# Optimization experiments

Hardware: AMD Instinct MI355X
Metric: run time of the kernel (lower is better)

## Reference

```python
import jax, jax.numpy as jnp
import numpy as np

NQ = 14            # n_qubits
NB = 2             # n_blocks
KLOC = 4           # k_local
K = 2 ** KLOC      # Hermitian observable dim = 16
NOFF = K * (K - 1) // 2   # 120 off-diagonal params
DEPTH = 3          # vqc_depth
IN_DIM = 784
OUT_DIM = 10
BATCH = 128
GROUPS = [list(range(s, s + KLOC)) for s in range(NQ - KLOC + 1)]  # sliding k-local groups
NOBS = len(GROUPS)  # 11
TOTAL_ENC = NB * ((NQ // 2) + ((NQ - 1) // 2)) * 15  # 390 SU(4) encoding params

# 15 two-qubit Pauli words in PennyLane's lexicographic IXYZ order (identity excluded)
_I = np.eye(2, dtype=np.complex64)
_X = np.array([[0, 1], [1, 0]], np.complex64)
_Y = np.array([[0, -1j], [1j, 0]], np.complex64)
_Z = np.array([[1, 0], [0, -1]], np.complex64)
_P = {'I': _I, 'X': _X, 'Y': _Y, 'Z': _Z}
_WORDS = [a + b for a in 'IXYZ' for b in 'IXYZ'][1:]
P15 = jnp.asarray(np.stack([np.kron(_P[w[0]], _P[w[1]]) for w in _WORDS]))  # (15,4,4)
CNOT = jnp.asarray(np.array([[1, 0, 0, 0], [0, 1, 0, 0], [0, 0, 0, 1], [0, 0, 1, 0]], np.complex64))
_ROWS, _COLS = np.tril_indices(K, -1)  # row-major lower-tri order == create_Hermitian fill order


def su4(theta):
    """PennyLane SpecialUnitary: U = expm(i * sum_m theta_m P_m), theta: (B,15).
    The generator is Hermitian, so use eigh instead of generic expm."""
    Hm = jnp.einsum('bm,mij->bij', theta.astype(jnp.complex64), P15)  # (B,4,4) Hermitian
    w, V = jnp.linalg.eigh(Hm)
    return jnp.einsum('bij,bj,bkj->bik', V, jnp.exp(1j * w.astype(jnp.complex64)), V.conj())


def apply_gate(state, U, wires):
    """Apply a k-qubit gate U ((B,2^k,2^k) or (2^k,2^k)) to state (B, 2,...,2)."""
    n = state.ndim - 1
    k = len(wires)
    axes = [w + 1 for w in wires]
    perm = [0] + axes + [a for a in range(1, n + 1) if a not in axes]
    st = jnp.transpose(state, perm)
    shp = st.shape
    st = st.reshape(shp[0], 2 ** k, -1)
    if U.ndim == 3:
        st = jnp.einsum('bij,bjr->bir', U, st)
    else:
        st = jnp.einsum('ij,bjr->bir', U, st)
    return jnp.transpose(st.reshape(shp), np.argsort(perm))


def expval_herm(state, H, wires):
    """<psi| H_{wires} |psi> per batch element."""
    n = state.ndim - 1
    axes = [w + 1 for w in wires]
    perm = [0] + axes + [a for a in range(1, n + 1) if a not in axes]
    st = jnp.transpose(state, perm).reshape(state.shape[0], H.shape[0], -1)
    return jnp.einsum('bkr,kl,blr->b', st.conj(), H, st).real


def create_hermitian(A, Bp, D):
    """Faithful port of create_Hermitian: lower-tri A+iB (row-major), diag D[1:] on
    positions 0..K-2 (D[0] unused, last diag 0), then H = h + h^dagger (diag doubled)."""
    h = jnp.zeros((K, K), jnp.complex64).at[_ROWS, _COLS].set(A + 1j * Bp)
    d = jnp.zeros((K,), A.dtype).at[jnp.arange(K - 1)].set(D[1:])
    h = h + jnp.diag(d).astype(jnp.complex64)
    return h + h.conj().T


def ry_mat(theta):
    c = jnp.cos(theta / 2)
    s = jnp.sin(theta / 2)
    return jnp.stack([jnp.stack([c, -s]), jnp.stack([s, c])]).astype(jnp.complex64)


def setup_inputs():
    key = jax.random.key(0)
    ks = jax.random.split(key, 9)
    lim = 1.0 / np.sqrt(IN_DIM)
    lim_h = 1.0 / np.sqrt(NOBS)
    return {
        'x': jax.random.normal(ks[0], (BATCH, IN_DIM), jnp.float32),
        'W_enc': jax.random.uniform(ks[1], (TOTAL_ENC, IN_DIM), jnp.float32, -lim, lim),
        'b_enc': jax.random.uniform(ks[2], (TOTAL_ENC,), jnp.float32, -lim, lim),
        'var_params': 0.01 * jax.random.normal(ks[3], (DEPTH, NQ), jnp.float32),
        'A': 2.0 * jax.random.normal(ks[4], (NOBS, NOFF), jnp.float32),
        'Bp': 2.0 * jax.random.normal(ks[5], (NOBS, NOFF), jnp.float32),
        'D': 2.0 * jax.random.normal(ks[6], (NOBS, K), jnp.float32),
        'W_head': jax.random.uniform(ks[7], (OUT_DIM, NOBS), jnp.float32, -lim_h, lim_h),
        'b_head': jax.random.uniform(ks[8], (OUT_DIM,), jnp.float32, -lim_h, lim_h),
    }


def reference(x, W_enc, b_enc, var_params, A, Bp, D, W_head, b_head):
    encoded = x @ W_enc.T + b_enc                      # (B, 390)
    Hs = jax.vmap(create_hermitian)(A, Bp, D)          # (NOBS, K, K)
    Bsz = x.shape[0]
    state = jnp.zeros((Bsz,) + (2,) * NQ, jnp.complex64).at[(slice(None),) + (0,) * NQ].set(1.0)
    # SU(4) brick-layer encoding: even pairs then odd pairs per block
    idx = 0
    for _ in range(NB):
        for q in list(range(0, NQ - 1, 2)) + list(range(1, NQ - 1, 2)):
            state = apply_gate(state, su4(encoded[:, idx:idx + 15]), [q, q + 1])
            idx += 15
    # variational RY + CNOT brick layers
    for layer in range(DEPTH):
        for q in range(NQ):
            state = apply_gate(state, ry_mat(var_params[layer, q]), [q])
        for q in list(range(0, NQ - 1, 2)) + list(range(1, NQ - 1, 2)):
            state = apply_gate(state, CNOT, [q, q + 1])
    q_out = jnp.stack([expval_herm(state, Hs[w], GROUPS[w]) for w in range(NOBS)], axis=1)
    q_out = q_out.astype(jnp.float32)                  # (B, NOBS)
    return q_out @ W_head.T + b_head                   # (B, OUT_DIM)
```

## Files before the change

kernel.cpp:

```cpp
#include <hip/hip_runtime.h>
#include <math.h>

#define NQ      14
#define NSTATE  16384
#define BATCH   128
#define DEPTH   3
#define NOBS    11
#define KDIM    16
#define NOFF    120
#define INDIM   784
#define OUTDIM  10

__device__ __forceinline__ int F2(int a) { return a + (a >> 4); }
#define PHYS2 (NSTATE + (NSTATE >> 4))

__device__ __forceinline__ float sbc(float x) {
  return __int_as_float(__builtin_amdgcn_readfirstlane(__float_as_int(x)));
}

__global__ __launch_bounds__(256) void enc_kernel(
    const float* __restrict__ x, const float* __restrict__ W,
    const float* __restrict__ bvec, float* __restrict__ theta)
{
  int wave = ((blockIdx.x << 2) | (threadIdx.x >> 6));
  int lane = threadIdx.x & 63;
  int g = wave >> 7;
  int b = wave & 127;

  const float4* x4 = (const float4*)(x + (size_t)b * INDIM);
  const float4* w4 = (const float4*)(W + (size_t)g * 15 * INDIM);

  float acc[15];
#pragma unroll
  for (int m = 0; m < 15; ++m) acc[m] = 0.f;
#pragma unroll
  for (int it = 0; it < 4; ++it) {
    int j4 = lane + it * 64;
    if (j4 < 196) {
      float4 xv = x4[j4];
#pragma unroll
      for (int m = 0; m < 15; ++m) {
        float4 wv = w4[m * 196 + j4];
        acc[m] = fmaf(xv.x, wv.x, fmaf(xv.y, wv.y, fmaf(xv.z, wv.z, fmaf(xv.w, wv.w, acc[m]))));
      }
    }
  }
#pragma unroll
  for (int m = 0; m < 15; ++m) {
#pragma unroll
    for (int off = 32; off; off >>= 1) acc[m] += __shfl_xor(acc[m], off);
  }
  if (lane == 0) {
#pragma unroll
    for (int m = 0; m < 15; ++m) theta[(size_t)wave * 15 + m] = acc[m] + bvec[g * 15 + m];
  }
}

__global__ __launch_bounds__(256) void expm_kernel(
    const float* __restrict__ theta, float2* __restrict__ Ubuf)
{
  int gid  = blockIdx.x * 256 + threadIdx.x;
  int pair = gid >> 2;
  int j    = gid & 3;
  int lane = threadIdx.x & 63;
  int grp  = lane & 60;

  const float* th = theta + (size_t)pair * 15;

  const float pr_[4][4] = {{1,0,0,1},{0,1,1,0},{0,0,0,0},{1,0,0,-1}};
  const float pi_[4][4] = {{0,0,0,0},{0,0,0,0},{0,-1,1,0},{0,0,0,0}};

  float Hre[16], Him[16];
#pragma unroll
  for (int e = 0; e < 16; ++e) { Hre[e] = 0.f; Him[e] = 0.f; }
  float tsum = 0.f;
#pragma unroll
  for (int m = 0; m < 15; ++m) {
    float tv = th[m];
    tsum += fabsf(tv);
    const int code = m + 1;
    const int a = code >> 2, c = code & 3;
#pragma unroll
    for (int i = 0; i < 4; ++i)
#pragma unroll
      for (int jj = 0; jj < 4; ++jj) {
        float ar = pr_[a][(i >> 1) * 2 + (jj >> 1)], ai = pi_[a][(i >> 1) * 2 + (jj >> 1)];
        float br = pr_[c][(i & 1) * 2 + (jj & 1)],   bi = pi_[c][(i & 1) * 2 + (jj & 1)];
        Hre[i * 4 + jj] += tv * (ar * br - ai * bi);
        Him[i * 4 + jj] += tv * (ar * bi + ai * br);
      }
  }
  int s = 0;
  if (tsum > 0.25f) {
    s = (int)ceilf(log2f(tsum * 4.0f));
    if (s < 0) s = 0;
    if (s > 14) s = 14;
  }
  float sc = exp2f((float)(-s));
  float Gre[16], Gim[16];
#pragma unroll
  for (int e = 0; e < 16; ++e) { Gre[e] = -Him[e] * sc; Gim[e] = Hre[e] * sc; }

  float Tcr[4], Tci[4];
#pragma unroll
  for (int i = 0; i < 4; ++i) {
    Tcr[i] = Gre[i * 4 + j] * (1.f / 9.f) + ((i == j) ? 1.f : 0.f);
    Tci[i] = Gim[i * 4 + j] * (1.f / 9.f);
  }
#pragma unroll
  for (int k = 8; k >= 1; --k) {
    float nr[4], ni[4];
    float invk = 1.0f / (float)k;
#pragma unroll
    for (int i = 0; i < 4; ++i) {
      float xr = 0.f, xi = 0.f;
#pragma unroll
      for (int l = 0; l < 4; ++l) {
        xr = fmaf(Gre[i * 4 + l], Tcr[l], fmaf(-Gim[i * 4 + l], Tci[l], xr));
        xi = fmaf(Gre[i * 4 + l], Tci[l], fmaf( Gim[i * 4 + l], Tcr[l], xi));
      }
      nr[i] = invk * xr + ((i == j) ? 1.f : 0.f);
      ni[i] = invk * xi;
    }
#pragma unroll
    for (int i = 0; i < 4; ++i) { Tcr[i] = nr[i]; Tci[i] = ni[i]; }
  }
  for (int it = 0; it < s; ++it) {
    float nr[4] = {0.f, 0.f, 0.f, 0.f}, ni[4] = {0.f, 0.f, 0.f, 0.f};
#pragma unroll
    for (int l = 0; l < 4; ++l) {
      int src = grp | l;
      float tlr = Tcr[l], tli = Tci[l];
#pragma unroll
      for (int i = 0; i < 4; ++i) {
        float br = __shfl(Tcr[i], src);
        float bi = __shfl(Tci[i], src);
        nr[i] = fmaf(br, tlr, fmaf(-bi, tli, nr[i]));
        ni[i] = fmaf(br, tli, fmaf( bi, tlr, ni[i]));
      }
    }
#pragma unroll
    for (int i = 0; i < 4; ++i) { Tcr[i] = nr[i]; Tci[i] = ni[i]; }
  }
#pragma unroll
  for (int i = 0; i < 4; ++i)
    Ubuf[(size_t)pair * 16 + i * 4 + j] = make_float2(Tcr[i], Tci[i]);
}

template<int S>
__device__ __forceinline__ int grpbase(int t) {
  return ((t >> S) << (S + 4)) | (t & ((1 << S) - 1));
}
template<int S>
__device__ __forceinline__ void ldgrp(const float2* st, int base, float* vr, float* vi) {
#pragma unroll
  for (int k = 0; k < 16; ++k) {
    float2 v = st[F2(base + (k << S))];
    vr[k] = v.x; vi[k] = v.y;
  }
}
template<int S>
__device__ __forceinline__ void stgrp(float2* st, int base, const float* vr, const float* vi) {
#pragma unroll
  for (int k = 0; k < 16; ++k) st[F2(base + (k << S))] = make_float2(vr[k], vi[k]);
}
__device__ __forceinline__ int base2s(int t) {
  return ((t >> 7) << 11) | (((t >> 5) & 3) << 7) | (t & 31);
}
__device__ __forceinline__ int addr2s(int base, int k) {
  return base + ((k >> 2) << 9) + ((k & 3) << 5);
}
__device__ __forceinline__ void ldgrp2(const float2* st, int base, float* vr, float* vi) {
#pragma unroll
  for (int k = 0; k < 16; ++k) {
    float2 v = st[F2(addr2s(base, k))];
    vr[k] = v.x; vi[k] = v.y;
  }
}
__device__ __forceinline__ void stgrp2(float2* st, int base, const float* vr, const float* vi) {
#pragma unroll
  for (int k = 0; k < 16; ++k) st[F2(addr2s(base, k))] = make_float2(vr[k], vi[k]);
}

__device__ __forceinline__ void loadU(const float2* __restrict__ Ug, float* ur, float* ui) {
#pragma unroll
  for (int e = 0; e < 16; ++e) {
    float2 u = Ug[e];
    ur[e] = sbc(u.x); ui[e] = sbc(u.y);
  }
}

__device__ __forceinline__ void applyU_hi(float* vr, float* vi, const float* ur, const float* ui) {
#pragma unroll
  for (int j2 = 0; j2 < 4; ++j2) {
    float ar[4], ai[4];
#pragma unroll
    for (int j = 0; j < 4; ++j) { ar[j] = vr[4 * j + j2]; ai[j] = vi[4 * j + j2]; }
#pragma unroll
    for (int i = 0; i < 4; ++i) {
      float xr = 0.f, xi = 0.f;
#pragma unroll
      for (int j = 0; j < 4; ++j) {
        xr = fmaf(ur[4 * i + j], ar[j], fmaf(-ui[4 * i + j], ai[j], xr));
        xi = fmaf(ur[4 * i + j], ai[j], fmaf( ui[4 * i + j], ar[j], xi));
      }
      vr[4 * i + j2] = xr; vi[4 * i + j2] = xi;
    }
  }
}
__device__ __forceinline__ void applyU_lo(float* vr, float* vi, const float* ur, const float* ui) {
#pragma unroll
  for (int i2 = 0; i2 < 4; ++i2) {
    float ar[4], ai[4];
#pragma unroll
    for (int j = 0; j < 4; ++j) { ar[j] = vr[4 * i2 + j]; ai[j] = vi[4 * i2 + j]; }
#pragma unroll
    for (int i = 0; i < 4; ++i) {
      float xr = 0.f, xi = 0.f;
#pragma unroll
      for (int j = 0; j < 4; ++j) {
        xr = fmaf(ur[4 * i + j], ar[j], fmaf(-ui[4 * i + j], ai[j], xr));
        xi = fmaf(ur[4 * i + j], ai[j], fmaf( ui[4 * i + j], ar[j], xi));
      }
      vr[4 * i2 + i] = xr; vi[4 * i2 + i] = xi;
    }
  }
}
__device__ __forceinline__ void applyU_mid(float* vr, float* vi, const float* ur, const float* ui) {
#pragma unroll
  for (int o = 0; o < 4; ++o) {
    const int kb = ((o >> 1) << 3) | (o & 1);
    float ar[4], ai[4];
#pragma unroll
    for (int j = 0; j < 4; ++j) { ar[j] = vr[kb | (j << 1)]; ai[j] = vi[kb | (j << 1)]; }
#pragma unroll
    for (int i = 0; i < 4; ++i) {
      float xr = 0.f, xi = 0.f;
#pragma unroll
      for (int j = 0; j < 4; ++j) {
        xr = fmaf(ur[4 * i + j], ar[j], fmaf(-ui[4 * i + j], ai[j], xr));
        xi = fmaf(ur[4 * i + j], ai[j], fmaf( ui[4 * i + j], ar[j], xi));
      }
      vr[kb | (i << 1)] = xr; vi[kb | (i << 1)] = xi;
    }
  }
}

template<int B>
__device__ __forceinline__ void ry16(float* vr, float* vi, float c, float s) {
#pragma unroll
  for (int k = 0; k < 16; ++k) {
    if (!(k & (1 << B))) {
      const int k1 = k | (1 << B);
      float r0 = vr[k], i0 = vi[k], r1 = vr[k1], i1 = vi[k1];
      vr[k]  = fmaf(c, r0, -s * r1);  vi[k]  = fmaf(c, i0, -s * i1);
      vr[k1] = fmaf(s, r0,  c * r1);  vi[k1] = fmaf(s, i0,  c * i1);
    }
  }
}
template<int CB, int TB>
__device__ __forceinline__ void cx16(float* vr, float* vi) {
#pragma unroll
  for (int k = 0; k < 16; ++k) {
    if ((k & (1 << CB)) && !(k & (1 << TB))) {
      const int k1 = k | (1 << TB);
      float tr = vr[k]; vr[k] = vr[k1]; vr[k1] = tr;
      float ti = vi[k]; vi[k] = vi[k1]; vi[k1] = ti;
    }
  }
}

template<int S>
__device__ __forceinline__ void enc_pass3(float2* st, const float2* __restrict__ U,
                                          int gHi, int gLo, int gMid, int b, int t) {
  float ur[16], ui[16], vr[16], vi[16];
  int base = grpbase<S>(t);
  ldgrp<S>(st, base, vr, vi);
  loadU(U + ((size_t)gHi  * BATCH + b) * 16, ur, ui); applyU_hi (vr, vi, ur, ui);
  loadU(U + ((size_t)gLo  * BATCH + b) * 16, ur, ui); applyU_lo (vr, vi, ur, ui);
  loadU(U + ((size_t)gMid * BATCH + b) * 16, ur, ui); applyU_mid(vr, vi, ur, ui);
  stgrp<S>(st, base, vr, vi);
}
__device__ __forceinline__ void enc_passD(float2* st, const float2* __restrict__ U,
                                          int gLo, int gMid, int b, int t) {
  float ur[16], ui[16], vr[16], vi[16];
  int base = t << 4;
  ldgrp<0>(st, base, vr, vi);
  loadU(U + ((size_t)gLo  * BATCH + b) * 16, ur, ui); applyU_lo (vr, vi, ur, ui);
  loadU(U + ((size_t)gMid * BATCH + b) * 16, ur, ui); applyU_mid(vr, vi, ur, ui);
  stgrp<0>(st, base, vr, vi);
}
__device__ __forceinline__ void enc_passE(float2* st, const float2* __restrict__ U,
                                          int gA, int gB, int b, int t) {
  float ur[16], ui[16], vr[16], vi[16];
  int base = base2s(t);
  ldgrp2(st, base, vr, vi);
  loadU(U + ((size_t)gA * BATCH + b) * 16, ur, ui); applyU_hi(vr, vi, ur, ui);
  loadU(U + ((size_t)gB * BATCH + b) * 16, ur, ui); applyU_lo(vr, vi, ur, ui);
  stgrp2(st, base, vr, vi);
}
template<int S>
__device__ __forceinline__ void var_pass3(float2* st, const float* __restrict__ vp,
                                          int l, int qbase, int t) {
  float vr[16], vi[16];
  int base = grpbase<S>(t);
  ldgrp<S>(st, base, vr, vi);
  float c[4], sn[4];
#pragma unroll
  for (int i = 0; i < 4; ++i) {
    float a = sbc(vp[l * NQ + qbase + i]) * 0.5f;
    c[i] = cosf(a); sn[i] = sinf(a);
  }
  ry16<3>(vr, vi, c[0], sn[0]);
  ry16<2>(vr, vi, c[1], sn[1]);
  ry16<1>(vr, vi, c[2], sn[2]);
  ry16<0>(vr, vi, c[3], sn[3]);
  cx16<3, 2>(vr, vi);
  cx16<1, 0>(vr, vi);
  cx16<2, 1>(vr, vi);
  stgrp<S>(st, base, vr, vi);
}
__device__ __forceinline__ void var_passD(float2* st, const float* __restrict__ vp,
                                          int l, int t) {
  float vr[16], vi[16];
  int base = t << 4;
  ldgrp<0>(st, base, vr, vi);
  float a0 = sbc(vp[l * NQ + 12]) * 0.5f;
  float a1 = sbc(vp[l * NQ + 13]) * 0.5f;
  ry16<1>(vr, vi, cosf(a0), sinf(a0));
  ry16<0>(vr, vi, cosf(a1), sinf(a1));
  cx16<1, 0>(vr, vi);
  cx16<2, 1>(vr, vi);
  stgrp<0>(st, base, vr, vi);
}
__device__ __forceinline__ void var_passE(float2* st, int t) {
  float vr[16], vi[16];
  int base = base2s(t);
  ldgrp2(st, base, vr, vi);
  cx16<3, 2>(vr, vi);
  cx16<1, 0>(vr, vi);
  stgrp2(st, base, vr, vi);
}

__global__ __launch_bounds__(1024) void qsim_kernel(
    const float2* __restrict__ U, const float* __restrict__ var_params,
    const float* __restrict__ A, const float* __restrict__ Bp,
    const float* __restrict__ D, const float* __restrict__ Wh,
    const float* __restrict__ bh, float* __restrict__ out)
{
  __shared__ float2 st[PHYS2];
  __shared__ float obsb[256];
  __shared__ float red[16];
  __shared__ float qv[NOBS];

  const int t = threadIdx.x;
  const int b = blockIdx.x;

  for (int i = t; i < PHYS2; i += 1024) st[i] = make_float2(0.f, 0.f);
  __syncthreads();
  if (t == 0) st[0] = make_float2(1.f, 0.f);
  __syncthreads();

  for (int nb = 0; nb < 2; ++nb) {
    int gI = nb * 13;
    enc_pass3<10>(st, U, gI + 0, gI + 1, gI + 7,  b, t); __syncthreads();
    enc_pass3<6 >(st, U, gI + 2, gI + 3, gI + 9,  b, t); __syncthreads();
    enc_pass3<2 >(st, U, gI + 4, gI + 5, gI + 11, b, t); __syncthreads();
    enc_passD    (st, U, gI + 6, gI + 12,         b, t); __syncthreads();
    enc_passE    (st, U, gI + 8, gI + 10,         b, t); __syncthreads();
  }

  for (int l = 0; l < DEPTH; ++l) {
    var_pass3<10>(st, var_params, l, 0, t); __syncthreads();
    var_pass3<6 >(st, var_params, l, 4, t); __syncthreads();
    var_pass3<2 >(st, var_params, l, 8, t); __syncthreads();
    var_passD    (st, var_params, l,    t); __syncthreads();
    var_passE    (st, t);                   __syncthreads();
  }

  for (int w = 0; w < NOBS; ++w) {
    if (t < NOFF) obsb[t] = A[w * NOFF + t];
    else if (t < 2 * NOFF) obsb[t] = Bp[w * NOFF + (t - NOFF)];
    else if (t < 2 * NOFF + KDIM) obsb[t] = D[w * KDIM + (t - 2 * NOFF)];
    __syncthreads();

    int shift = 10 - w;
    int hi = t >> shift;
    int lo = t & ((1 << shift) - 1);
    int base2 = (hi << (shift + 4)) | lo;
    float sr[16], si[16];
#pragma unroll
    for (int k = 0; k < 16; ++k) {
      float2 v = st[F2(base2 + (k << shift))];
      sr[k] = v.x; si[k] = v.y;
    }
    float E = 0.f;
#pragma unroll
    for (int k = 0; k < 15; ++k)
      E = fmaf(obsb[240 + k + 1], sr[k] * sr[k] + si[k] * si[k], E);
#pragma unroll
    for (int k = 1; k < 16; ++k) {
#pragma unroll
      for (int l2 = 0; l2 < k; ++l2) {
        const int pidx = (k * (k - 1)) / 2 + l2;
        float t1 = sr[k] * sr[l2] + si[k] * si[l2];
        float t2 = si[k] * sr[l2] - sr[k] * si[l2];
        E = fmaf(obsb[pidx], t1, fmaf(obsb[NOFF + pidx], t2, E));
      }
    }
    E *= 2.0f;
#pragma unroll
    for (int off = 32; off; off >>= 1) E += __shfl_xor(E, off);
    if ((t & 63) == 0) red[t >> 6] = E;
    __syncthreads();
    if (t == 0) {
      float sum = 0.f;
      for (int ww = 0; ww < 16; ++ww) sum += red[ww];
      qv[w] = sum;
    }
    __syncthreads();
  }

  if (t < OUTDIM) {
    float o = bh[t];
#pragma unroll
    for (int w = 0; w < NOBS; ++w) o = fmaf(Wh[t * NOBS + w], qv[w], o);
    out[b * OUTDIM + t] = o;
  }
}

extern "C" void kernel_launch(void* const* d_in, const int* in_sizes, int n_in,
                              void* d_out, int out_size, void* d_ws, size_t ws_size,
                              hipStream_t stream) {
  const float* x          = (const float*)d_in[0];
  const float* W_enc      = (const float*)d_in[1];
  const float* b_enc      = (const float*)d_in[2];
  const float* var_params = (const float*)d_in[3];
  const float* A          = (const float*)d_in[4];
  const float* Bp         = (const float*)d_in[5];
  const float* D          = (const float*)d_in[6];
  const float* W_head     = (const float*)d_in[7];
  const float* b_head     = (const float*)d_in[8];
  float* out = (float*)d_out;

  float*  theta = (float*)d_ws;
  size_t  thBytes = (size_t)3328 * 15 * sizeof(float);
  float2* Ubuf = (float2*)((char*)d_ws + ((thBytes + 255) / 256) * 256);

  enc_kernel <<<832, 256, 0, stream>>>(x, W_enc, b_enc, theta);
  expm_kernel<<<52,  256, 0, stream>>>(theta, Ubuf);
  qsim_kernel<<<128, 1024, 0, stream>>>(Ubuf, var_params, A, Bp, D,
                                        W_head, b_head, out);
}
```

Baseline: 207.4 us.

## Duplicate state simulation across two blocks per sample, split observables, atomically combine

Launches two blocks per batch element, each redoing the full state-vector simulation and then evaluating half of the 11 observables. Partial head outputs are combined with atomicAdd into an output zeroed by a memset. Observable parameters are preloaded once and the per-observable syncs are removed. The aim is to fill more of the GPU's CUs, at the cost of doubling the simulation work and adding a memset launch.

```diff
diff --git a/kernel.cpp b/kernel.cpp
--- a/kernel.cpp
+++ b/kernel.cpp
@@ -349,16 +349,16 @@
     const float* __restrict__ bh, float* __restrict__ out)
 {
   __shared__ float2 st[PHYS2];
-  __shared__ float obsb[256];
-  __shared__ float red[16];
-  __shared__ float qv[NOBS];
+  __shared__ float obsa[6 * 256];
+  __shared__ float red[6][16];
 
   const int t = threadIdx.x;
-  const int b = blockIdx.x;
-
-  for (int i = t; i < PHYS2; i += 1024) st[i] = make_float2(0.f, 0.f);
-  __syncthreads();
-  if (t == 0) st[0] = make_float2(1.f, 0.f);
+  const int b = blockIdx.x >> 1;
+  const int h = blockIdx.x & 1;
+  const int nw = h ? 5 : 6;
+
+  for (int i = t; i < PHYS2; i += 1024)
+    st[i] = (i == 0) ? make_float2(1.f, 0.f) : make_float2(0.f, 0.f);
   __syncthreads();
 
   for (int nb = 0; nb < 2; ++nb) {
@@ -378,16 +378,25 @@
     var_passE    (st, t);                   __syncthreads();
   }
 
-  for (int w = 0; w < NOBS; ++w) {
-    if (t < NOFF) obsb[t] = A[w * NOFF + t];
-    else if (t < 2 * NOFF) obsb[t] = Bp[w * NOFF + (t - NOFF)];
-    else if (t < 2 * NOFF + KDIM) obsb[t] = D[w * KDIM + (t - 2 * NOFF)];
-    __syncthreads();
-
+  for (int i = t; i < nw * 256; i += 1024) {
+    int idx = i >> 8, off = i & 255, w = 2 * idx + h;
+    float v;
+    if (off < NOFF)            v = A[w * NOFF + off];
+    else if (off < 2 * NOFF)   v = Bp[w * NOFF + (off - NOFF)];
+    else if (off < 2 * NOFF + KDIM) v = D[w * KDIM + (off - 2 * NOFF)];
+    else v = 0.f;
+    obsa[i] = v;
+  }
+  __syncthreads();
+
+  const int wave = t >> 6;
+  for (int idx = 0; idx < nw; ++idx) {
+    const int w = 2 * idx + h;
+    const float* ob = &obsa[idx << 8];
     int shift = 10 - w;
-    int hi = t >> shift;
+    int hi2 = t >> shift;
     int lo = t & ((1 << shift) - 1);
-    int base2 = (hi << (shift + 4)) | lo;
+    int base2 = (hi2 << (shift + 4)) | lo;
     float sr[16], si[16];
 #pragma unroll
     for (int k = 0; k < 16; ++k) {
@@ -397,7 +406,7 @@
     float E = 0.f;
 #pragma unroll
     for (int k = 0; k < 15; ++k)
-      E = fmaf(obsb[240 + k + 1], sr[k] * sr[k] + si[k] * si[k], E);
+      E = fmaf(ob[240 + k + 1], sr[k] * sr[k] + si[k] * si[k], E);
 #pragma unroll
     for (int k = 1; k < 16; ++k) {
 #pragma unroll
@@ -405,27 +414,26 @@
         const int pidx = (k * (k - 1)) / 2 + l2;
         float t1 = sr[k] * sr[l2] + si[k] * si[l2];
         float t2 = si[k] * sr[l2] - sr[k] * si[l2];
-        E = fmaf(obsb[pidx], t1, fmaf(obsb[NOFF + pidx], t2, E));
+        E = fmaf(ob[pidx], t1, fmaf(ob[NOFF + pidx], t2, E));
       }
     }
     E *= 2.0f;
 #pragma unroll
     for (int off = 32; off; off >>= 1) E += __shfl_xor(E, off);
-    if ((t & 63) == 0) red[t >> 6] = E;
-    __syncthreads();
-    if (t == 0) {
-      float sum = 0.f;
-      for (int ww = 0; ww < 16; ++ww) sum += red[ww];
-      qv[w] = sum;
-    }
-    __syncthreads();
-  }
+    if ((t & 63) == 0) red[idx][wave] = E;
+  }
+  __syncthreads();
 
   if (t < OUTDIM) {
-    float o = bh[t];
-#pragma unroll
-    for (int w = 0; w < NOBS; ++w) o = fmaf(Wh[t * NOBS + w], qv[w], o);
-    out[b * OUTDIM + t] = o;
+    float o = (h == 0) ? bh[t] : 0.f;
+    for (int idx = 0; idx < nw; ++idx) {
+      const int w = 2 * idx + h;
+      float q = 0.f;
+#pragma unroll
+      for (int ww = 0; ww < 16; ++ww) q += red[idx][ww];
+      o = fmaf(Wh[t * NOBS + w], q, o);
+    }
+    atomicAdd(&out[b * OUTDIM + t], o);
   }
 }
 
@@ -447,8 +455,9 @@
   size_t  thBytes = (size_t)3328 * 15 * sizeof(float);
   float2* Ubuf = (float2*)((char*)d_ws + ((thBytes + 255) / 256) * 256);
 
+  hipMemsetAsync(out, 0, (size_t)out_size * sizeof(float), stream);
   enc_kernel <<<832, 256, 0, stream>>>(x, W_enc, b_enc, theta);
   expm_kernel<<<52,  256, 0, stream>>>(theta, Ubuf);
-  qsim_kernel<<<128, 1024, 0, stream>>>(Ubuf, var_params, A, Bp, D,
+  qsim_kernel<<<256, 1024, 0, stream>>>(Ubuf, var_params, A, Bp, D,
                                         W_head, b_head, out);
 }
```

Result: faster. 182.1 us (-12.2%).
